# Kernel tuning notes

Measured on AMD Instinct MI355X. Metric: run time of the kernel, lower is better.

Reference implementation:

```python
import jax, jax.numpy as jnp
import numpy as np

DIM = 1024
HEADS = 16
WIN = 128          # local window size
BATCH = 4
SEQ = 4096
HEAD_DIM = DIM // HEADS
HIDDEN = 2 * DIM   # GEGLU hidden_dim = 2*dim
EPS = 1e-5
NEG_INF = -1e9


def layer_norm(x, g, b):
    m = jnp.mean(x, axis=-1, keepdims=True)
    v = jnp.mean((x - m) ** 2, axis=-1, keepdims=True)
    return (x - m) * jax.lax.rsqrt(v + EPS) * g + b


def sliding_causal_local_attn(x, wq, wk, wv, wo, bo, rel_bias):
    # x: [B, S, D]; sliding-window causal attention: each query attends to
    # its own window plus the previous window (look_backward=1), causally masked.
    B, S, D = x.shape
    h, w, dh = HEADS, WIN, HEAD_DIM
    nw = S // w
    scale = dh ** -0.5

    def split_heads(t):  # [B,S,D] -> [B,h,nw,w,dh]
        return t.reshape(B, S, h, dh).transpose(0, 2, 1, 3).reshape(B, h, nw, w, dh)

    q = split_heads(x @ wq)
    k = split_heads(x @ wk)
    v = split_heads(x @ wv)

    # context = [previous window ; current window] -> [B,h,nw,2w,dh]
    k_pad = jnp.pad(k, ((0, 0), (0, 0), (1, 0), (0, 0), (0, 0)))
    v_pad = jnp.pad(v, ((0, 0), (0, 0), (1, 0), (0, 0), (0, 0)))
    kc = jnp.concatenate([k_pad[:, :, :-1], k_pad[:, :, 1:]], axis=3)
    vc = jnp.concatenate([v_pad[:, :, :-1], v_pad[:, :, 1:]], axis=3)

    logits = jnp.einsum('bhnid,bhnjd->bhnij', q, kc) * scale  # [B,h,nw,w,2w]

    i = jnp.arange(w)[:, None]        # query pos within window
    j = jnp.arange(2 * w)[None, :]    # key pos within [prev;cur] context
    dist = i + w - j                  # relative distance, 0..2w-1 when causal
    causal = dist >= 0
    # learned relative position bias per head, indexed by distance
    bias = rel_bias[:, jnp.clip(dist, 0, 2 * w - 1)]  # [h, w, 2w]
    logits = logits + bias[None, :, None]

    n_idx = jnp.arange(nw)[:, None, None]
    valid = causal[None] & ((n_idx > 0) | (j[None] >= w))  # mask padded first window
    logits = jnp.where(valid[None, None], logits, NEG_INF)

    attn = jax.nn.softmax(logits, axis=-1)
    out = jnp.einsum('bhnij,bhnjd->bhnid', attn, vc)           # [B,h,nw,w,dh]
    out = out.reshape(B, h, S, dh).transpose(0, 2, 1, 3).reshape(B, S, D)
    return out @ wo + bo


def geglu(x, w1, b1, w2, b2):
    proj = x @ w1 + b1                         # [B,S,2*HIDDEN]
    val, gate = jnp.split(proj, 2, axis=-1)
    return (val * jax.nn.gelu(gate, approximate=False)) @ w2 + b2


def setup_inputs() -> dict:
    key = jax.random.key(0)
    ks = jax.random.split(key, 12)
    sd = 0.02
    return {
        'x': jax.random.normal(ks[0], (BATCH, SEQ, DIM), jnp.float32),
        'ln1_g': jnp.ones((DIM,), jnp.float32),
        'ln1_b': jnp.zeros((DIM,), jnp.float32),
        'ln2_g': jnp.ones((DIM,), jnp.float32),
        'ln2_b': jnp.zeros((DIM,), jnp.float32),
        'wq': jax.random.normal(ks[1], (DIM, DIM), jnp.float32) * sd,
        'wk': jax.random.normal(ks[2], (DIM, DIM), jnp.float32) * sd,
        'wv': jax.random.normal(ks[3], (DIM, DIM), jnp.float32) * sd,
        'wo': jax.random.normal(ks[4], (DIM, DIM), jnp.float32) * sd,
        'bo': jnp.zeros((DIM,), jnp.float32),
        'rel_bias': jax.random.normal(ks[5], (HEADS, 2 * WIN), jnp.float32) * sd,
        'w_ff1': jax.random.normal(ks[6], (DIM, 2 * HIDDEN), jnp.float32) * sd,
        'b_ff1': jnp.zeros((2 * HIDDEN,), jnp.float32),
        'w_ff2': jax.random.normal(ks[7], (HIDDEN, DIM), jnp.float32) * sd,
        'b_ff2': jnp.zeros((DIM,), jnp.float32),
    }


def reference(x, ln1_g, ln1_b, ln2_g, ln2_b, wq, wk, wv, wo, bo, rel_bias,
              w_ff1, b_ff1, w_ff2, b_ff2):
    x = x + sliding_causal_local_attn(layer_norm(x, ln1_g, ln1_b),
                                      wq, wk, wv, wo, bo, rel_bias)
    x = x + geglu(layer_norm(x, ln2_g, ln2_b), w_ff1, b_ff1, w_ff2, b_ff2)
    return x
```

## Files before the change

kernel.cpp:

```cpp
#include <hip/hip_runtime.h>
#include <math.h>

typedef __attribute__((ext_vector_type(8))) short s16x8;
typedef __attribute__((ext_vector_type(4))) float f32x4;

__device__ __forceinline__ float b2f(unsigned short u){
  unsigned int i = ((unsigned int)u) << 16;
  float f; __builtin_memcpy(&f, &i, 4); return f;
}
__device__ __forceinline__ unsigned short f2b(float f){
  unsigned int i; __builtin_memcpy(&i, &f, 4);
  unsigned int r = (i + 0x7fffu + ((i >> 16) & 1u)) >> 16;
  return (unsigned short)r;
}
__device__ __forceinline__ f32x4 mfma16(s16x8 a, s16x8 b, f32x4 c){
  return __builtin_amdgcn_mfma_f32_16x16x32_bf16(a, b, c, 0, 0, 0);
}
__device__ __forceinline__ float gelu_exact(float x){
  return 0.5f * x * (1.0f + erff(x * 0.70710678118654752f));
}
__device__ __forceinline__ void gl_lds16(const unsigned short* g, unsigned short* l){
  __builtin_amdgcn_global_load_lds(
      (const __attribute__((address_space(1))) unsigned int*)g,
      (__attribute__((address_space(3))) unsigned int*)l, 16, 0, 0);
}

__device__ __forceinline__ void ln_row(const float* __restrict__ xrow,
                                       const float* __restrict__ g,
                                       const float* __restrict__ b,
                                       unsigned short* __restrict__ orow, int lane){
  const float4* xr = (const float4*)xrow;
  float4 u[4];
  #pragma unroll
  for(int q = 0; q < 4; q++) u[q] = xr[lane + 64*q];
  float s = 0.0f, ss = 0.0f;
  #pragma unroll
  for(int q = 0; q < 4; q++){
    s  += u[q].x + u[q].y + u[q].z + u[q].w;
    ss += u[q].x*u[q].x + u[q].y*u[q].y + u[q].z*u[q].z + u[q].w*u[q].w;
  }
  #pragma unroll
  for(int o = 32; o; o >>= 1){ s += __shfl_xor(s, o, 64); ss += __shfl_xor(ss, o, 64); }
  float m = s * (1.0f/1024.0f);
  float inv = rsqrtf(ss * (1.0f/1024.0f) - m*m + 1e-5f);
  #pragma unroll
  for(int q = 0; q < 4; q++){
    float4 ug = ((const float4*)g)[lane + 64*q];
    float4 ub = ((const float4*)b)[lane + 64*q];
    ushort4 o4;
    o4.x = f2b((u[q].x - m) * inv * ug.x + ub.x);
    o4.y = f2b((u[q].y - m) * inv * ug.y + ub.y);
    o4.z = f2b((u[q].z - m) * inv * ug.z + ub.z);
    o4.w = f2b((u[q].w - m) * inv * ug.w + ub.w);
    ((ushort4*)orow)[lane + 64*q] = o4;
  }
}

__global__ __launch_bounds__(256) void prep_k(
    const float* __restrict__ x, const float* __restrict__ ln1_g, const float* __restrict__ ln1_b,
    unsigned short* __restrict__ h,
    const float* __restrict__ wq, const float* __restrict__ wk, const float* __restrict__ wv,
    const float* __restrict__ wo, const float* __restrict__ wff1, const float* __restrict__ wff2,
    unsigned short* __restrict__ wqkvT, unsigned short* __restrict__ woT,
    unsigned short* __restrict__ wff1T, unsigned short* __restrict__ wff2T)
{
  const int bz = blockIdx.x;
  if(bz >= 10240){
    int id = bz - 10240;
    int lane = threadIdx.x & 63, wave = threadIdx.x >> 6;
    int row = id * 4 + wave;
    ln_row(x + (size_t)row*1024, ln1_g, ln1_b, h + (size_t)row*1024, lane);
    return;
  }
  const float* in; unsigned short* out; int R, C, c0, r0;
  if(bz < 4096){
    int w = bz >> 10, id = bz & 1023;
    const float* srcs[4] = {wq, wk, wv, wo};
    unsigned short* dsts[4] = {wqkvT, wqkvT + 1048576, wqkvT + 2097152, woT};
    in = srcs[w]; out = dsts[w]; R = 1024; C = 1024;
    c0 = (id & 31) * 32; r0 = (id >> 5) * 32;
  } else if(bz < 8192){
    int id = bz - 4096;
    in = wff1; out = wff1T; R = 1024; C = 4096;
    c0 = (id & 127) * 32; r0 = (id >> 7) * 32;
  } else {
    int id = bz - 8192;
    in = wff2; out = wff2T; R = 2048; C = 1024;
    c0 = (id & 31) * 32; r0 = (id >> 5) * 32;
  }
  __shared__ unsigned short tile[32][33];
  int tx = threadIdx.x & 31, ty = threadIdx.x >> 5;
  #pragma unroll
  for(int i = 0; i < 4; i++)
    tile[ty + 8*i][tx] = f2b(in[(size_t)(r0 + ty + 8*i) * C + c0 + tx]);
  __syncthreads();
  #pragma unroll
  for(int i = 0; i < 4; i++)
    out[(size_t)(c0 + ty + 8*i) * R + r0 + tx] = tile[tx][ty + 8*i];
}

__global__ __launch_bounds__(256) void ln2_k(const float* __restrict__ x,
                                             const float* __restrict__ g,
                                             const float* __restrict__ b,
                                             unsigned short* __restrict__ out){
  int lane = threadIdx.x & 63, wave = threadIdx.x >> 6;
  int row = blockIdx.x * 4 + wave;
  ln_row(x + (size_t)row*1024, g, b, out + (size_t)row*1024, lane);
}

template<int MODE>
__global__ __launch_bounds__(512, 1) void gemm256(
    const unsigned short* __restrict__ A, const unsigned short* __restrict__ Bt,
    void* Cv, void* Cv2, int N, int n_split, int K,
    const float* __restrict__ bias, const float* __restrict__ res, int ntpb)
{
  __shared__ __align__(16) unsigned short As[2][256*64];
  __shared__ __align__(16) unsigned short Bs[2][256*64];

  const int p = blockIdx.x;
  const int tid = threadIdx.x;
  const int wave = tid >> 6, lane = tid & 63;
  const int ln3 = lane >> 3;
  const int cg  = (lane & 7) ^ ln3;
  const int wm = (wave >> 2) * 128, wn = (wave & 3) * 64;
  const int lrow = lane & 15, quad = lane >> 4, xw = lrow & 7;
  const int nk = K >> 6;

  auto tmn = [&](int o, int& m0, int& n0){
    unsigned int lin = (unsigned int)p + ((unsigned int)o << 8);
    unsigned int xcd = lin & 7u, idx = lin >> 3;
    m0 = (int)(xcd * 8u + (idx & 7u)) * 256;
    n0 = (int)(idx >> 3) * (MODE == 1 ? 128 : 256);
  };

  const unsigned short* aP[4];
  const unsigned short* bP[4];
  auto setp = [&](int m0, int n0){
    #pragma unroll
    for(int hq = 0; hq < 4; hq++){
      int rt = hq*64 + wave*8 + ln3;
      aP[hq] = A + (size_t)(m0 + rt)*K + cg*8;
      int brow;
      if(MODE == 1){
        int grp = rt >> 4;
        brow = (grp & 1)*2048 + n0 + ((grp >> 1) << 4) + (rt & 15);
      } else {
        brow = n0 + rt;
      }
      bP[hq] = Bt + (size_t)brow*K + cg*8;
    }
  };

  int os = 0, ks = 0;
  auto adv = [&](){
    ++ks;
    if(ks == nk){
      ks = 0; ++os;
      if(os < ntpb){ int m0n, n0n; tmn(os, m0n, n0n); setp(m0n, n0n); }
    } else {
      aP[0] += 64; aP[1] += 64; aP[2] += 64; aP[3] += 64;
      bP[0] += 64; bP[1] += 64; bP[2] += 64; bP[3] += 64;
    }
  };

#define STAGE8(bsel) do{ \
    gl_lds16(aP[0], &As[bsel][             wave*512]); \
    gl_lds16(aP[1], &As[bsel][      4096 + wave*512]); \
    gl_lds16(aP[2], &As[bsel][ 8192      + wave*512]); \
    gl_lds16(aP[3], &As[bsel][ 8192+4096 + wave*512]); \
    gl_lds16(bP[0], &Bs[bsel][             wave*512]); \
    gl_lds16(bP[1], &Bs[bsel][      4096 + wave*512]); \
    gl_lds16(bP[2], &Bs[bsel][ 8192      + wave*512]); \
    gl_lds16(bP[3], &Bs[bsel][ 8192+4096 + wave*512]); \
  }while(0)
#define RD(buf, rowbase, kk) \
    (*(const s16x8*)&(buf)[((rowbase) + lrow)*64 + (((((kk)<<2)+quad)^xw)*8)])

  f32x4 acc[8][4];
  #pragma unroll
  for(int i = 0; i < 8; i++)
    #pragma unroll
    for(int j = 0; j < 4; j++)
      #pragma unroll
      for(int r = 0; r < 4; r++) acc[i][j][r] = 0.0f;

  int m0c, n0c; tmn(0, m0c, n0c);
  int oc = 0, ktc = 0;

  setp(m0c, n0c);
  STAGE8(0);
  adv();

  s16x8 af[4], bfv[4][2];
  const int tot = ntpb * nk;
  for(int j = 0; j < tot; ++j){
    const int cur = j & 1, nxt = cur ^ 1;
    if(j + 1 < tot){
      STAGE8(nxt);
      asm volatile("s_waitcnt vmcnt(8)\n\ts_barrier" ::: "memory");
      adv();
    } else {
      asm volatile("s_waitcnt vmcnt(0)\n\ts_barrier" ::: "memory");
    }

    const unsigned short* bA = &As[cur][0];
    const unsigned short* bB = &Bs[cur][0];
    #pragma unroll
    for(int half = 0; half < 2; half++){
      const int rb = wm + half*64;
      #pragma unroll
      for(int kk = 0; kk < 2; kk++){
        #pragma unroll
        for(int i = 0; i < 4; i++) af[i] = RD(bA, rb + i*16, kk);
        if(half == 0){
          #pragma unroll
          for(int j4 = 0; j4 < 4; j4++) bfv[j4][kk] = RD(bB, wn + j4*16, kk);
        }
        __builtin_amdgcn_s_setprio(1);
        #pragma unroll
        for(int i = 0; i < 4; i++)
          #pragma unroll
          for(int j4 = 0; j4 < 4; j4++)
            acc[half*4 + i][j4] = mfma16(af[i], bfv[j4][kk], acc[half*4 + i][j4]);
        __builtin_amdgcn_s_setprio(0);
      }
    }
    asm volatile("s_waitcnt lgkmcnt(0)\n\ts_barrier" ::: "memory");

    ++ktc;
    if(ktc == nk){
      ktc = 0;
      const int qr = quad * 4;
      if(MODE == 1){
        unsigned short* C = (unsigned short*)Cv;
        const int a4 = wave & 3;
        #pragma unroll
        for(int i = 0; i < 8; i++){
          #pragma unroll
          for(int gp = 0; gp < 2; gp++){
            int colv = n0c + a4*32 + gp*16 + lrow;
            float bv = bias[colv];
            float bg = bias[2048 + colv];
            #pragma unroll
            for(int r = 0; r < 4; r++){
              size_t row = (size_t)(m0c + wm + i*16 + qr + r);
              float v  = acc[i][2*gp  ][r] + bv;
              float gt = acc[i][2*gp+1][r] + bg;
              C[row*2048 + colv] = f2b(v * gelu_exact(gt));
            }
          }
        }
      } else if(MODE == 0){
        const bool left = (n0c + 256) <= n_split;
        unsigned short* Cb = left ? (unsigned short*)Cv : (unsigned short*)Cv2;
        const int stride = left ? n_split : (N - n_split);
        const int cb0 = left ? n0c : (n0c - n_split);
        #pragma unroll
        for(int i = 0; i < 8; i++)
          #pragma unroll
          for(int j4 = 0; j4 < 4; j4++){
            int col = cb0 + wn + j4*16 + lrow;
            #pragma unroll
            for(int r = 0; r < 4; r++){
              size_t row = (size_t)(m0c + wm + i*16 + qr + r);
              Cb[row*stride + col] = f2b(acc[i][j4][r]);
            }
          }
      } else {
        float* C = (float*)Cv;
        #pragma unroll
        for(int i = 0; i < 8; i++)
          #pragma unroll
          for(int j4 = 0; j4 < 4; j4++){
            int col = n0c + wn + j4*16 + lrow;
            float bv = bias[col];
            #pragma unroll
            for(int r = 0; r < 4; r++){
              size_t row = (size_t)(m0c + wm + i*16 + qr + r);
              size_t idx = row * (size_t)N + col;
              C[idx] = acc[i][j4][r] + bv + res[idx];
            }
          }
      }
      #pragma unroll
      for(int i = 0; i < 8; i++)
        #pragma unroll
        for(int j4 = 0; j4 < 4; j4++)
          #pragma unroll
          for(int r = 0; r < 4; r++) acc[i][j4][r] = 0.0f;
      ++oc;
      if(oc < ntpb) tmn(oc, m0c, n0c);
    }
  }
#undef STAGE8
#undef RD
}

__global__ __launch_bounds__(256, 1) void attn_k(const unsigned short* __restrict__ qk,
                                                 const unsigned short* __restrict__ vbuf,
                                                 const float* __restrict__ rel_bias,
                                                 unsigned short* __restrict__ attn_out)
{
  __shared__ unsigned short kvS[128 * 72];
  __shared__ unsigned short PS[128 * 136];
  __shared__ float biasS[256];

  const int n = blockIdx.x, h = blockIdx.y, b = blockIdx.z;
  const int tid = threadIdx.x;
  const int wave = tid >> 6, lane = tid & 63;
  const int lrow = lane & 15, quad = lane >> 4, lk = quad * 8;
  const int rbase = wave * 32;
  const size_t rowbase = (size_t)b * 4096;
  const int prev = (n > 0) ? (n - 1) : 0;

  biasS[tid] = rel_bias[h * 256 + tid];

  s16x8 aq[2][2];
  #pragma unroll
  for(int mi = 0; mi < 2; mi++)
    #pragma unroll
    for(int kk = 0; kk < 2; kk++)
      aq[mi][kk] = *(const s16x8*)&qk[(rowbase + n*128 + rbase + mi*16 + lrow)*2048
                                      + h*64 + kk*32 + lk];

  f32x4 lg[2][16];
  #pragma unroll
  for(int mi = 0; mi < 2; mi++)
    #pragma unroll
    for(int nj = 0; nj < 16; nj++)
      #pragma unroll
      for(int r = 0; r < 4; r++) lg[mi][nj][r] = 0.0f;

  for(int jh = 0; jh < 2; jh++){
    if(jh) __syncthreads();
    #pragma unroll
    for(int it = 0; it < 4; it++){
      int cid = tid + it * 256;
      int jloc = cid >> 3, c8 = (cid & 7) * 8;
      int j = jh * 128 + jloc;
      int srow = (j < 128) ? (prev*128 + j) : (n*128 + j - 128);
      *(s16x8*)&kvS[jloc*72 + c8] =
        *(const s16x8*)&qk[(rowbase + srow)*2048 + 1024 + h*64 + c8];
    }
    __syncthreads();
    #pragma unroll
    for(int njl = 0; njl < 8; njl++){
      #pragma unroll
      for(int kk = 0; kk < 2; kk++){
        s16x8 bk = *(const s16x8*)&kvS[(njl*16 + lrow)*72 + kk*32 + lk];
        #pragma unroll
        for(int mi = 0; mi < 2; mi++)
          lg[mi][jh*8 + njl] = mfma16(aq[mi][kk], bk, lg[mi][jh*8 + njl]);
      }
    }
  }
  __syncthreads();

  #pragma unroll
  for(int mi = 0; mi < 2; mi++){
    #pragma unroll
    for(int r = 0; r < 4; r++){
      int i = rbase + mi*16 + quad*4 + r;
      float mx = -3e38f;
      #pragma unroll
      for(int nj = 0; nj < 16; nj++){
        int j = nj*16 + lrow;
        int dist = i + 128 - j;
        bool valid = (dist >= 0) && ((n > 0) || (j >= 128));
        float l = valid ? (lg[mi][nj][r] * 0.125f + biasS[dist & 255]) : -1e9f;
        lg[mi][nj][r] = l;
        mx = fmaxf(mx, l);
      }
      #pragma unroll
      for(int o = 1; o < 16; o <<= 1) mx = fmaxf(mx, __shfl_xor(mx, o, 64));
      float s = 0.0f;
      #pragma unroll
      for(int nj = 0; nj < 16; nj++){
        float p = __expf(lg[mi][nj][r] - mx);
        lg[mi][nj][r] = p;
        s += p;
      }
      #pragma unroll
      for(int o = 1; o < 16; o <<= 1) s += __shfl_xor(s, o, 64);
      float inv = 1.0f / s;
      #pragma unroll
      for(int nj = 0; nj < 16; nj++) lg[mi][nj][r] *= inv;
    }
  }

  f32x4 o_acc[2][4];
  #pragma unroll
  for(int mi = 0; mi < 2; mi++)
    #pragma unroll
    for(int nj = 0; nj < 4; nj++)
      #pragma unroll
      for(int r = 0; r < 4; r++) o_acc[mi][nj][r] = 0.0f;

  for(int jh = 0; jh < 2; jh++){
    {
      int jloc = tid >> 1;
      int dbase = (tid & 1) * 32;
      int j = jh * 128 + jloc;
      int srow = (j < 128) ? (prev*128 + j) : (n*128 + j - 128);
      const unsigned short* vr = &vbuf[(rowbase + srow)*1024 + h*64 + dbase];
      #pragma unroll
      for(int i8 = 0; i8 < 4; i8++){
        s16x8 vv = *(const s16x8*)&vr[i8 * 8];
        #pragma unroll
        for(int e = 0; e < 8; e++)
          kvS[(dbase + i8*8 + e)*136 + jloc] = (unsigned short)vv[e];
      }
    }
    #pragma unroll
    for(int mi = 0; mi < 2; mi++)
      #pragma unroll
      for(int r = 0; r < 4; r++)
        #pragma unroll
        for(int njl = 0; njl < 8; njl++)
          PS[(rbase + mi*16 + quad*4 + r)*136 + njl*16 + lrow] = f2b(lg[mi][jh*8 + njl][r]);
    __syncthreads();
    #pragma unroll
    for(int kk = 0; kk < 4; kk++){
      s16x8 ap[2];
      #pragma unroll
      for(int mi = 0; mi < 2; mi++)
        ap[mi] = *(const s16x8*)&PS[(rbase + mi*16 + lrow)*136 + kk*32 + lk];
      #pragma unroll
      for(int nj = 0; nj < 4; nj++){
        s16x8 bv = *(const s16x8*)&kvS[(nj*16 + lrow)*136 + kk*32 + lk];
        #pragma unroll
        for(int mi = 0; mi < 2; mi++)
          o_acc[mi][nj] = mfma16(ap[mi], bv, o_acc[mi][nj]);
      }
    }
    __syncthreads();
  }

  #pragma unroll
  for(int mi = 0; mi < 2; mi++)
    #pragma unroll
    for(int nj = 0; nj < 4; nj++)
      #pragma unroll
      for(int r = 0; r < 4; r++){
        size_t row = rowbase + n*128 + rbase + mi*16 + quad*4 + r;
        int col = h*64 + nj*16 + lrow;
        attn_out[row * 1024 + col] = f2b(o_acc[mi][nj][r]);
      }
}

extern "C" void kernel_launch(void* const* d_in, const int* in_sizes, int n_in,
                              void* d_out, int out_size, void* d_ws, size_t ws_size,
                              hipStream_t stream) {
  const float* x     = (const float*)d_in[0];
  const float* ln1_g = (const float*)d_in[1];
  const float* ln1_b = (const float*)d_in[2];
  const float* ln2_g = (const float*)d_in[3];
  const float* ln2_b = (const float*)d_in[4];
  const float* wq    = (const float*)d_in[5];
  const float* wk    = (const float*)d_in[6];
  const float* wv    = (const float*)d_in[7];
  const float* wo    = (const float*)d_in[8];
  const float* bo    = (const float*)d_in[9];
  const float* rel   = (const float*)d_in[10];
  const float* wff1  = (const float*)d_in[11];
  const float* bff1  = (const float*)d_in[12];
  const float* wff2  = (const float*)d_in[13];
  const float* bff2  = (const float*)d_in[14];
  float* out = (float*)d_out;
  char*  ws  = (char*)d_ws;

  unsigned short* wqkvT = (unsigned short*)(ws);
  unsigned short* woT   = (unsigned short*)(ws +  6291456);
  unsigned short* wff1T = (unsigned short*)(ws +  8388608);
  unsigned short* wff2T = (unsigned short*)(ws + 16777216);
  unsigned short* h     = (unsigned short*)(ws + 20971520);
  unsigned short* qk    = (unsigned short*)(ws + 54525952);
  unsigned short* ff    = qk;
  unsigned short* vbuf  = (unsigned short*)d_out;
  float*          x1    = out;

  prep_k<<<14336, 256, 0, stream>>>(x, ln1_g, ln1_b, h,
                                    wq, wk, wv, wo, wff1, wff2,
                                    wqkvT, woT, wff1T, wff2T);
  gemm256<0><<<256, 512, 0, stream>>>(h, wqkvT, qk, vbuf, 3072, 2048, 1024,
                                      nullptr, nullptr, 3);
  attn_k<<<dim3(32, 16, 4), 256, 0, stream>>>(qk, vbuf, rel, h);
  gemm256<2><<<256, 512, 0, stream>>>(h, woT, x1, nullptr, 1024, 0, 1024,
                                      bo, x, 1);
  ln2_k<<<4096, 256, 0, stream>>>(x1, ln2_g, ln2_b, h);
  gemm256<1><<<256, 512, 0, stream>>>(h, wff1T, ff, nullptr, 2048, 0, 1024,
                                      bff1, nullptr, 4);
  gemm256<2><<<256, 512, 0, stream>>>(ff, wff2T, out, nullptr, 1024, 0, 2048,
                                      bff2, x1, 1);
}
```

Measured before the change: 740.6 us.

## Switch GEMM to 32x32 MFMA, stream B directly from global, halve LDS

The shared GEMM kernel now uses 32x32x16 bf16 MFMA with 16-wide accumulators instead of 16x16x32. It no longer stages the B tile in LDS: each wave reads its B fragments straight from global memory. Only A is double-buffered through LDS, which halves shared memory and lets launch bounds request two blocks per CU. The aim is to cut LDS traffic, free occupancy and use the larger MFMA shape. The risk is extra global-load latency on B fragments, which now sit on the critical path with no prefetch.

```diff
diff --git a/kernel.cpp b/kernel.cpp
--- a/kernel.cpp
+++ b/kernel.cpp
@@ -3,6 +3,7 @@
 
 typedef __attribute__((ext_vector_type(8))) short s16x8;
 typedef __attribute__((ext_vector_type(4))) float f32x4;
+typedef __attribute__((ext_vector_type(16))) float f32x16;
 
 __device__ __forceinline__ float b2f(unsigned short u){
   unsigned int i = ((unsigned int)u) << 16;
@@ -15,6 +16,9 @@
 }
 __device__ __forceinline__ f32x4 mfma16(s16x8 a, s16x8 b, f32x4 c){
   return __builtin_amdgcn_mfma_f32_16x16x32_bf16(a, b, c, 0, 0, 0);
+}
+__device__ __forceinline__ f32x16 mfma32(s16x8 a, s16x8 b, f32x16 c){
+  return __builtin_amdgcn_mfma_f32_32x32x16_bf16(a, b, c, 0, 0, 0);
 }
 __device__ __forceinline__ float gelu_exact(float x){
   return 0.5f * x * (1.0f + erff(x * 0.70710678118654752f));
@@ -109,13 +113,12 @@
 }
 
 template<int MODE>
-__global__ __launch_bounds__(512, 1) void gemm256(
+__global__ __launch_bounds__(512, 2) void gemm256(
     const unsigned short* __restrict__ A, const unsigned short* __restrict__ Bt,
     void* Cv, void* Cv2, int N, int n_split, int K,
     const float* __restrict__ bias, const float* __restrict__ res, int ntpb)
 {
   __shared__ __align__(16) unsigned short As[2][256*64];
-  __shared__ __align__(16) unsigned short Bs[2][256*64];
 
   const int p = blockIdx.x;
   const int tid = threadIdx.x;
@@ -123,7 +126,7 @@
   const int ln3 = lane >> 3;
   const int cg  = (lane & 7) ^ ln3;
   const int wm = (wave >> 2) * 128, wn = (wave & 3) * 64;
-  const int lrow = lane & 15, quad = lane >> 4, xw = lrow & 7;
+  const int l31 = lane & 31, hi = lane >> 5, x7 = lane & 7;
   const int nk = K >> 6;
 
   auto tmn = [&](int o, int& m0, int& n0){
@@ -134,166 +137,156 @@
   };
 
   const unsigned short* aP[4];
-  const unsigned short* bP[4];
-  auto setp = [&](int m0, int n0){
+  auto setp = [&](int m0){
     #pragma unroll
     for(int hq = 0; hq < 4; hq++){
       int rt = hq*64 + wave*8 + ln3;
       aP[hq] = A + (size_t)(m0 + rt)*K + cg*8;
-      int brow;
-      if(MODE == 1){
-        int grp = rt >> 4;
-        brow = (grp & 1)*2048 + n0 + ((grp >> 1) << 4) + (rt & 15);
-      } else {
-        brow = n0 + rt;
-      }
-      bP[hq] = Bt + (size_t)brow*K + cg*8;
     }
   };
-
-  int os = 0, ks = 0;
+  const unsigned short* pB[2];
+  auto setb = [&](int n0){
+    #pragma unroll
+    for(int nj = 0; nj < 2; nj++){
+      int bRow;
+      if(MODE == 1) bRow = nj*2048 + n0 + (wave & 3)*32 + l31;
+      else          bRow = n0 + wn + nj*32 + l31;
+      pB[nj] = Bt + (size_t)bRow*K + hi*8;
+    }
+  };
+
+  int os = 0, ks_ = 0;
   auto adv = [&](){
-    ++ks;
-    if(ks == nk){
-      ks = 0; ++os;
-      if(os < ntpb){ int m0n, n0n; tmn(os, m0n, n0n); setp(m0n, n0n); }
+    ++ks_;
+    if(ks_ == nk){
+      ks_ = 0; ++os;
+      if(os < ntpb){ int m0n, n0n; tmn(os, m0n, n0n); setp(m0n); }
     } else {
       aP[0] += 64; aP[1] += 64; aP[2] += 64; aP[3] += 64;
-      bP[0] += 64; bP[1] += 64; bP[2] += 64; bP[3] += 64;
     }
   };
 
-#define STAGE8(bsel) do{ \
-    gl_lds16(aP[0], &As[bsel][             wave*512]); \
-    gl_lds16(aP[1], &As[bsel][      4096 + wave*512]); \
-    gl_lds16(aP[2], &As[bsel][ 8192      + wave*512]); \
-    gl_lds16(aP[3], &As[bsel][ 8192+4096 + wave*512]); \
-    gl_lds16(bP[0], &Bs[bsel][             wave*512]); \
-    gl_lds16(bP[1], &Bs[bsel][      4096 + wave*512]); \
-    gl_lds16(bP[2], &Bs[bsel][ 8192      + wave*512]); \
-    gl_lds16(bP[3], &Bs[bsel][ 8192+4096 + wave*512]); \
+#define STAGE4(bsel) do{ \
+    gl_lds16(aP[0], &As[bsel][        wave*512]); \
+    gl_lds16(aP[1], &As[bsel][ 4096 + wave*512]); \
+    gl_lds16(aP[2], &As[bsel][ 8192 + wave*512]); \
+    gl_lds16(aP[3], &As[bsel][12288 + wave*512]); \
   }while(0)
-#define RD(buf, rowbase, kk) \
-    (*(const s16x8*)&(buf)[((rowbase) + lrow)*64 + (((((kk)<<2)+quad)^xw)*8)])
-
-  f32x4 acc[8][4];
-  #pragma unroll
-  for(int i = 0; i < 8; i++)
-    #pragma unroll
-    for(int j = 0; j < 4; j++)
-      #pragma unroll
-      for(int r = 0; r < 4; r++) acc[i][j][r] = 0.0f;
+
+  f32x16 acc[4][2];
+  #pragma unroll
+  for(int i = 0; i < 4; i++)
+    #pragma unroll
+    for(int jn = 0; jn < 2; jn++)
+      #pragma unroll
+      for(int r = 0; r < 16; r++) acc[i][jn][r] = 0.0f;
 
   int m0c, n0c; tmn(0, m0c, n0c);
   int oc = 0, ktc = 0;
 
-  setp(m0c, n0c);
-  STAGE8(0);
+  setp(m0c);
+  setb(n0c);
+  STAGE4(0);
   adv();
 
-  s16x8 af[4], bfv[4][2];
   const int tot = ntpb * nk;
   for(int j = 0; j < tot; ++j){
     const int cur = j & 1, nxt = cur ^ 1;
     if(j + 1 < tot){
-      STAGE8(nxt);
-      asm volatile("s_waitcnt vmcnt(8)\n\ts_barrier" ::: "memory");
+      STAGE4(nxt);
+      asm volatile("s_waitcnt vmcnt(4)\n\ts_barrier" ::: "memory");
       adv();
     } else {
       asm volatile("s_waitcnt vmcnt(0)\n\ts_barrier" ::: "memory");
     }
 
     const unsigned short* bA = &As[cur][0];
-    const unsigned short* bB = &Bs[cur][0];
-    #pragma unroll
-    for(int half = 0; half < 2; half++){
-      const int rb = wm + half*64;
-      #pragma unroll
-      for(int kk = 0; kk < 2; kk++){
-        #pragma unroll
-        for(int i = 0; i < 4; i++) af[i] = RD(bA, rb + i*16, kk);
-        if(half == 0){
-          #pragma unroll
-          for(int j4 = 0; j4 < 4; j4++) bfv[j4][kk] = RD(bB, wn + j4*16, kk);
-        }
-        __builtin_amdgcn_s_setprio(1);
-        #pragma unroll
-        for(int i = 0; i < 4; i++)
-          #pragma unroll
-          for(int j4 = 0; j4 < 4; j4++)
-            acc[half*4 + i][j4] = mfma16(af[i], bfv[j4][kk], acc[half*4 + i][j4]);
-        __builtin_amdgcn_s_setprio(0);
-      }
-    }
+    #pragma unroll
+    for(int ks = 0; ks < 4; ks++){
+      const int csw = (((ks*2 + hi) ^ x7) * 8);
+      s16x8 af0 = *(const s16x8*)&bA[(wm +  0 + l31)*64 + csw];
+      s16x8 af1 = *(const s16x8*)&bA[(wm + 32 + l31)*64 + csw];
+      s16x8 af2 = *(const s16x8*)&bA[(wm + 64 + l31)*64 + csw];
+      s16x8 af3 = *(const s16x8*)&bA[(wm + 96 + l31)*64 + csw];
+      s16x8 bg0 = *(const s16x8*)(pB[0] + ks*16);
+      s16x8 bg1 = *(const s16x8*)(pB[1] + ks*16);
+      __builtin_amdgcn_s_setprio(1);
+      acc[0][0] = mfma32(af0, bg0, acc[0][0]);
+      acc[0][1] = mfma32(af0, bg1, acc[0][1]);
+      acc[1][0] = mfma32(af1, bg0, acc[1][0]);
+      acc[1][1] = mfma32(af1, bg1, acc[1][1]);
+      acc[2][0] = mfma32(af2, bg0, acc[2][0]);
+      acc[2][1] = mfma32(af2, bg1, acc[2][1]);
+      acc[3][0] = mfma32(af3, bg0, acc[3][0]);
+      acc[3][1] = mfma32(af3, bg1, acc[3][1]);
+      __builtin_amdgcn_s_setprio(0);
+    }
+    pB[0] += 64; pB[1] += 64;
     asm volatile("s_waitcnt lgkmcnt(0)\n\ts_barrier" ::: "memory");
 
     ++ktc;
     if(ktc == nk){
       ktc = 0;
-      const int qr = quad * 4;
       if(MODE == 1){
         unsigned short* C = (unsigned short*)Cv;
-        const int a4 = wave & 3;
-        #pragma unroll
-        for(int i = 0; i < 8; i++){
+        const int colv = n0c + (wave & 3)*32 + l31;
+        const float bv = bias[colv];
+        const float bg = bias[2048 + colv];
+        #pragma unroll
+        for(int mi = 0; mi < 4; mi++)
           #pragma unroll
-          for(int gp = 0; gp < 2; gp++){
-            int colv = n0c + a4*32 + gp*16 + lrow;
-            float bv = bias[colv];
-            float bg = bias[2048 + colv];
-            #pragma unroll
-            for(int r = 0; r < 4; r++){
-              size_t row = (size_t)(m0c + wm + i*16 + qr + r);
-              float v  = acc[i][2*gp  ][r] + bv;
-              float gt = acc[i][2*gp+1][r] + bg;
-              C[row*2048 + colv] = f2b(v * gelu_exact(gt));
-            }
+          for(int r = 0; r < 16; r++){
+            int rowl = (r & 3) + 8*(r >> 2) + 4*hi;
+            size_t row = (size_t)(m0c + wm + mi*32 + rowl);
+            float v = acc[mi][0][r] + bv;
+            float g = acc[mi][1][r] + bg;
+            C[row*2048 + colv] = f2b(v * gelu_exact(g));
           }
-        }
       } else if(MODE == 0){
         const bool left = (n0c + 256) <= n_split;
         unsigned short* Cb = left ? (unsigned short*)Cv : (unsigned short*)Cv2;
         const int stride = left ? n_split : (N - n_split);
         const int cb0 = left ? n0c : (n0c - n_split);
         #pragma unroll
-        for(int i = 0; i < 8; i++)
+        for(int mi = 0; mi < 4; mi++)
           #pragma unroll
-          for(int j4 = 0; j4 < 4; j4++){
-            int col = cb0 + wn + j4*16 + lrow;
+          for(int nj = 0; nj < 2; nj++){
+            int col = cb0 + wn + nj*32 + l31;
             #pragma unroll
-            for(int r = 0; r < 4; r++){
-              size_t row = (size_t)(m0c + wm + i*16 + qr + r);
-              Cb[row*stride + col] = f2b(acc[i][j4][r]);
+            for(int r = 0; r < 16; r++){
+              int rowl = (r & 3) + 8*(r >> 2) + 4*hi;
+              size_t row = (size_t)(m0c + wm + mi*32 + rowl);
+              Cb[row*stride + col] = f2b(acc[mi][nj][r]);
             }
           }
       } else {
         float* C = (float*)Cv;
         #pragma unroll
-        for(int i = 0; i < 8; i++)
+        for(int mi = 0; mi < 4; mi++)
           #pragma unroll
-          for(int j4 = 0; j4 < 4; j4++){
-            int col = n0c + wn + j4*16 + lrow;
+          for(int nj = 0; nj < 2; nj++){
+            int col = n0c + wn + nj*32 + l31;
             float bv = bias[col];
             #pragma unroll
-            for(int r = 0; r < 4; r++){
-              size_t row = (size_t)(m0c + wm + i*16 + qr + r);
+            for(int r = 0; r < 16; r++){
+              int rowl = (r & 3) + 8*(r >> 2) + 4*hi;
+              size_t row = (size_t)(m0c + wm + mi*32 + rowl);
               size_t idx = row * (size_t)N + col;
-              C[idx] = acc[i][j4][r] + bv + res[idx];
+              C[idx] = acc[mi][nj][r] + bv + res[idx];
             }
           }
       }
       #pragma unroll
-      for(int i = 0; i < 8; i++)
-        #pragma unroll
-        for(int j4 = 0; j4 < 4; j4++)
+      for(int i = 0; i < 4; i++)
+        #pragma unroll
+        for(int jn = 0; jn < 2; jn++)
           #pragma unroll
-          for(int r = 0; r < 4; r++) acc[i][j4][r] = 0.0f;
+          for(int r = 0; r < 16; r++) acc[i][jn][r] = 0.0f;
       ++oc;
-      if(oc < ntpb) tmn(oc, m0c, n0c);
-    }
-  }
-#undef STAGE8
-#undef RD
+      if(oc < ntpb){ tmn(oc, m0c, n0c); setb(n0c); }
+    }
+  }
+#undef STAGE4
 }
 
 __global__ __launch_bounds__(256, 1) void attn_k(const unsigned short* __restrict__ qk,
```

New measurement: 999.0 us. +34.9%, slower.

## Split GEMM inner loop into four barrier-synchronized LDS-read/MFMA quadrant phases

Applied to the files above, without the earlier changes.

Restructures the per-k-step compute of the persistent GEMM into four phases over 2x2 output quadrants. Each phase has its own LDS fragment loads, workgroup barriers, sched_barrier fences and setprio-bracketed MFMA bursts, in the style of ping-pong scheduling. The goal is to keep the waves in lockstep so that LDS reads and MFMA issue overlap better across waves. In exchange it adds many more s_barrier calls per k-step, which may cost more than the overlap gains, and it changes register pressure for the fragment buffers.

```diff
diff --git a/kernel.cpp b/kernel.cpp
--- a/kernel.cpp
+++ b/kernel.cpp
@@ -151,11 +151,11 @@
     }
   };
 
-  int os = 0, ks = 0;
+  int os = 0, ks_ = 0;
   auto adv = [&](){
-    ++ks;
-    if(ks == nk){
-      ks = 0; ++os;
+    ++ks_;
+    if(ks_ == nk){
+      ks_ = 0; ++os;
       if(os < ntpb){ int m0n, n0n; tmn(os, m0n, n0n); setp(m0n, n0n); }
     } else {
       aP[0] += 64; aP[1] += 64; aP[2] += 64; aP[3] += 64;
@@ -191,41 +191,94 @@
   STAGE8(0);
   adv();
 
-  s16x8 af[4], bfv[4][2];
+  s16x8 af[4], bf0[2][2], bf1[2][2];
   const int tot = ntpb * nk;
   for(int j = 0; j < tot; ++j){
     const int cur = j & 1, nxt = cur ^ 1;
     if(j + 1 < tot){
       STAGE8(nxt);
-      asm volatile("s_waitcnt vmcnt(8)\n\ts_barrier" ::: "memory");
+      asm volatile("s_waitcnt vmcnt(8)" ::: "memory");
       adv();
     } else {
-      asm volatile("s_waitcnt vmcnt(0)\n\ts_barrier" ::: "memory");
-    }
+      asm volatile("s_waitcnt vmcnt(0)" ::: "memory");
+    }
+    __builtin_amdgcn_s_barrier();
+    __builtin_amdgcn_sched_barrier(0);
 
     const unsigned short* bA = &As[cur][0];
     const unsigned short* bB = &Bs[cur][0];
-    #pragma unroll
-    for(int half = 0; half < 2; half++){
-      const int rb = wm + half*64;
-      #pragma unroll
-      for(int kk = 0; kk < 2; kk++){
-        #pragma unroll
-        for(int i = 0; i < 4; i++) af[i] = RD(bA, rb + i*16, kk);
-        if(half == 0){
-          #pragma unroll
-          for(int j4 = 0; j4 < 4; j4++) bfv[j4][kk] = RD(bB, wn + j4*16, kk);
-        }
-        __builtin_amdgcn_s_setprio(1);
-        #pragma unroll
-        for(int i = 0; i < 4; i++)
-          #pragma unroll
-          for(int j4 = 0; j4 < 4; j4++)
-            acc[half*4 + i][j4] = mfma16(af[i], bfv[j4][kk], acc[half*4 + i][j4]);
-        __builtin_amdgcn_s_setprio(0);
-      }
-    }
-    asm volatile("s_waitcnt lgkmcnt(0)\n\ts_barrier" ::: "memory");
+
+    #pragma unroll
+    for(int i = 0; i < 4; i++){ af[i] = RD(bA, wm + i*16, 0); }
+    s16x8 af1k[4];
+    #pragma unroll
+    for(int i = 0; i < 4; i++){ af1k[i] = RD(bA, wm + i*16, 1); }
+    #pragma unroll
+    for(int jj = 0; jj < 2; jj++){ bf0[jj][0] = RD(bB, wn + jj*16, 0);
+                                   bf0[jj][1] = RD(bB, wn + jj*16, 1); }
+    asm volatile("s_waitcnt lgkmcnt(8)" ::: "memory");
+    __builtin_amdgcn_s_barrier();
+    asm volatile("s_waitcnt lgkmcnt(0)" ::: "memory");
+    __builtin_amdgcn_sched_barrier(0);
+    __builtin_amdgcn_s_setprio(1);
+    #pragma unroll
+    for(int i = 0; i < 4; i++)
+      #pragma unroll
+      for(int jj = 0; jj < 2; jj++){
+        acc[i][jj] = mfma16(af[i],   bf0[jj][0], acc[i][jj]);
+        acc[i][jj] = mfma16(af1k[i], bf0[jj][1], acc[i][jj]);
+      }
+    __builtin_amdgcn_s_setprio(0);
+    __builtin_amdgcn_sched_barrier(0);
+    __builtin_amdgcn_s_barrier();
+
+    #pragma unroll
+    for(int jj = 0; jj < 2; jj++){ bf1[jj][0] = RD(bB, wn + 32 + jj*16, 0);
+                                   bf1[jj][1] = RD(bB, wn + 32 + jj*16, 1); }
+    __builtin_amdgcn_s_barrier();
+    asm volatile("s_waitcnt lgkmcnt(0)" ::: "memory");
+    __builtin_amdgcn_sched_barrier(0);
+    __builtin_amdgcn_s_setprio(1);
+    #pragma unroll
+    for(int i = 0; i < 4; i++)
+      #pragma unroll
+      for(int jj = 0; jj < 2; jj++){
+        acc[i][2+jj] = mfma16(af[i],   bf1[jj][0], acc[i][2+jj]);
+        acc[i][2+jj] = mfma16(af1k[i], bf1[jj][1], acc[i][2+jj]);
+      }
+    __builtin_amdgcn_s_setprio(0);
+    __builtin_amdgcn_sched_barrier(0);
+    __builtin_amdgcn_s_barrier();
+
+    #pragma unroll
+    for(int i = 0; i < 4; i++){ af[i]   = RD(bA, wm + 64 + i*16, 0);
+                                af1k[i] = RD(bA, wm + 64 + i*16, 1); }
+    __builtin_amdgcn_s_barrier();
+    asm volatile("s_waitcnt lgkmcnt(0)" ::: "memory");
+    __builtin_amdgcn_sched_barrier(0);
+    __builtin_amdgcn_s_setprio(1);
+    #pragma unroll
+    for(int i = 0; i < 4; i++)
+      #pragma unroll
+      for(int jj = 0; jj < 2; jj++){
+        acc[4+i][jj] = mfma16(af[i],   bf0[jj][0], acc[4+i][jj]);
+        acc[4+i][jj] = mfma16(af1k[i], bf0[jj][1], acc[4+i][jj]);
+      }
+    __builtin_amdgcn_s_setprio(0);
+    __builtin_amdgcn_sched_barrier(0);
+    __builtin_amdgcn_s_barrier();
+
+    __builtin_amdgcn_s_setprio(1);
+    #pragma unroll
+    for(int i = 0; i < 4; i++)
+      #pragma unroll
+      for(int jj = 0; jj < 2; jj++){
+        acc[4+i][2+jj] = mfma16(af[i],   bf1[jj][0], acc[4+i][2+jj]);
+        acc[4+i][2+jj] = mfma16(af1k[i], bf1[jj][1], acc[4+i][2+jj]);
+      }
+    __builtin_amdgcn_s_setprio(0);
+    __builtin_amdgcn_sched_barrier(0);
+    __builtin_amdgcn_s_barrier();
 
     ++ktc;
     if(ktc == nk){
@@ -258,12 +311,12 @@
         #pragma unroll
         for(int i = 0; i < 8; i++)
           #pragma unroll
-          for(int j4 = 0; j4 < 4; j4++){
-            int col = cb0 + wn + j4*16 + lrow;
+          for(int jj = 0; jj < 4; jj++){
+            int col = cb0 + wn + jj*16 + lrow;
             #pragma unroll
             for(int r = 0; r < 4; r++){
               size_t row = (size_t)(m0c + wm + i*16 + qr + r);
-              Cb[row*stride + col] = f2b(acc[i][j4][r]);
+              Cb[row*stride + col] = f2b(acc[i][jj][r]);
             }
           }
       } else {
@@ -271,23 +324,23 @@
         #pragma unroll
         for(int i = 0; i < 8; i++)
           #pragma unroll
-          for(int j4 = 0; j4 < 4; j4++){
-            int col = n0c + wn + j4*16 + lrow;
+          for(int jj = 0; jj < 4; jj++){
+            int col = n0c + wn + jj*16 + lrow;
             float bv = bias[col];
             #pragma unroll
             for(int r = 0; r < 4; r++){
               size_t row = (size_t)(m0c + wm + i*16 + qr + r);
               size_t idx = row * (size_t)N + col;
-              C[idx] = acc[i][j4][r] + bv + res[idx];
+              C[idx] = acc[i][jj][r] + bv + res[idx];
             }
           }
       }
       #pragma unroll
       for(int i = 0; i < 8; i++)
         #pragma unroll
-        for(int j4 = 0; j4 < 4; j4++)
+        for(int jj = 0; jj < 4; jj++)
           #pragma unroll
-          for(int r = 0; r < 4; r++) acc[i][j4][r] = 0.0f;
+          for(int r = 0; r < 4; r++) acc[i][jj][r] = 0.0f;
       ++oc;
       if(oc < ntpb) tmn(oc, m0c, n0c);
     }
```

New measurement: 783.2 us. 5.7% more time.
